# Kernel tuning notes

Hardware: AMD Instinct MI355X
Metric: run time of the kernel (lower is better)

The kernel has to match this reference:

```python
import jax, jax.numpy as jnp
import numpy as np

K = 10  # knn_graph default k
NEG_SLOPE = 0.2


def _knn_idx(x, k):
    # x: (B, N, C) -> idx (B, N, k) of nearest neighbors (excluding self)
    x2 = jnp.sum(x * x, axis=-1)                       # (B, N)
    d = x2[:, :, None] + x2[:, None, :] - 2.0 * jnp.einsum('bnc,bmc->bnm', x, x)
    _, idx = jax.lax.top_k(-d, k + 1)                  # smallest distances
    return idx[:, :, 1:]                               # drop self


def _edge_conv(x, W, s, t, k):
    # x: (B, N, C); W: (O, 2C); s,t: (O,) folded BN scale/bias
    idx = _knn_idx(x, k)                               # (B, N, k)
    neigh = jax.vmap(lambda xb, ib: xb[ib])(x, idx)    # (B, N, k, C)
    xi = jnp.broadcast_to(x[:, :, None, :], neigh.shape)
    edge = jnp.concatenate([neigh - xi, xi], axis=-1)  # (B, N, k, 2C)
    h = jnp.einsum('bnkc,oc->bnko', edge, W) * s + t
    h = jnp.where(h >= 0, h, NEG_SLOPE * h)            # LeakyReLU(0.2)
    return jnp.max(h, axis=2)                          # max over neighbors -> (B, N, O)


def setup_inputs() -> dict:
    key = jax.random.key(0)
    ks = jax.random.split(key, 32)
    B, N = 8, 2048
    NC = 3
    def w(k_, shape):
        fan_in = shape[-1]
        return jax.random.normal(k_, shape, jnp.float32) * (1.0 / np.sqrt(fan_in))
    def sb(k_, c):  # positive scale, small bias
        k1, k2 = jax.random.split(k_)
        return (jax.random.uniform(k1, (c,), jnp.float32, 0.5, 1.5),
                jax.random.normal(k2, (c,), jnp.float32) * 0.1)
    points = jax.random.normal(ks[0], (B, N, 3), jnp.float32)
    W1 = w(ks[1], (64, 6));    s1, t1 = sb(ks[2], 64)
    W2 = w(ks[3], (64, 128));  s2, t2 = sb(ks[4], 64)
    W3 = w(ks[5], (128, 128)); s3, t3 = sb(ks[6], 128)
    W4 = w(ks[7], (256, 256)); s4, t4 = sb(ks[8], 256)
    W5 = w(ks[9], (1024, 512)); s5, t5 = sb(ks[10], 1024)
    Wf1 = w(ks[11], (512, 1024)); sf1, tf1 = sb(ks[12], 512)
    Wf2 = w(ks[13], (256, 512)); bf2 = jax.random.normal(ks[14], (256,), jnp.float32) * 0.02
    sf2, tf2 = sb(ks[15], 256)
    Wf3 = w(ks[16], (NC, 256)); bf3 = jax.random.normal(ks[17], (NC,), jnp.float32) * 0.02
    return {
        'points': points,
        'W1': W1, 's1': s1, 't1': t1,
        'W2': W2, 's2': s2, 't2': t2,
        'W3': W3, 's3': s3, 't3': t3,
        'W4': W4, 's4': s4, 't4': t4,
        'W5': W5, 's5': s5, 't5': t5,
        'Wf1': Wf1, 'sf1': sf1, 'tf1': tf1,
        'Wf2': Wf2, 'bf2': bf2, 'sf2': sf2, 'tf2': tf2,
        'Wf3': Wf3, 'bf3': bf3,
    }


def reference(points, W1, s1, t1, W2, s2, t2, W3, s3, t3, W4, s4, t4,
              W5, s5, t5, Wf1, sf1, tf1, Wf2, bf2, sf2, tf2, Wf3, bf3):
    lrelu = lambda h: jnp.where(h >= 0, h, NEG_SLOPE * h)
    out1 = _edge_conv(points, W1, s1, t1, K)   # (B, N, 64)
    out2 = _edge_conv(out1, W2, s2, t2, K)     # (B, N, 64)
    out3 = _edge_conv(out2, W3, s3, t3, K)     # (B, N, 128)
    out4 = _edge_conv(out3, W4, s4, t4, K)     # (B, N, 256)
    x = jnp.concatenate([out1, out2, out3, out4], axis=-1)  # (B, N, 512)
    h = lrelu(jnp.einsum('bnc,oc->bno', x, W5) * s5 + t5)   # (B, N, 1024)
    h = jnp.max(h, axis=1)                                  # global max pool -> (B, 1024)
    h = lrelu((h @ Wf1.T) * sf1 + tf1)                      # (B, 512); dropout=identity (eval)
    h = lrelu((h @ Wf2.T + bf2) * sf2 + tf2)                # (B, 256)
    return h @ Wf3.T + bf3                                  # (B, num_classes)
```

## Files before the change

kernel.cpp:

```cpp
#include <hip/hip_runtime.h>
#include <hip/hip_bf16.h>


#define NEG 0.2f
#define FMAX 3.402823466e+38f
#define FMAXB 0x7F7FFFFFu
#define KINIT 0x7F7FFFFFFFFFFFFFull

typedef __hip_bfloat16 bf16;
typedef __attribute__((ext_vector_type(8))) short s8v;
typedef __attribute__((ext_vector_type(4))) float f32x4;
typedef unsigned long long u64;

#define BB 8
#define NN 2048
#define BNTOT (BB * NN)
#define NPART 4

#define OFF_NORMS ((size_t)0)
#define OFF_PART (OFF_NORMS + BNTOT)
#define OFF_POOLED (OFF_PART + 8 * 1024 * 32)
#define OFF_H1 (OFF_POOLED + 8 * 1024)
#define OFF_H2 (OFF_H1 + 8 * 512)
#define WSF_TOTAL (OFF_H2 + 8 * 256)

#define WB1 0
#define WB2 4096
#define WB3 12288
#define WB4 28672
#define WTOT 94208

__device__ float g_ws_f[WSF_TOTAL];
__device__ float g_G[(size_t)8 * BNTOT * 64];
__device__ u64 g_pk[(size_t)BNTOT * NPART * 10];
__device__ unsigned g_th[BNTOT];
__device__ int g_flag;
__device__ unsigned short g_hi[(size_t)BNTOT * 512];
__device__ unsigned short g_lo[(size_t)BNTOT * 512];
__device__ unsigned short g_xhi5[(size_t)BNTOT * 512];
__device__ unsigned short g_xlo5[(size_t)BNTOT * 512];
__device__ unsigned short g_whi[1024 * 512];
__device__ unsigned short g_wlo[1024 * 512];
__device__ unsigned short g_wfh[WTOT];
__device__ unsigned short g_wfl[WTOT];

__device__ __forceinline__ float ldany(const void* p, size_t i, int isb) {
  if (isb) return __bfloat162float(((const bf16*)p)[i]);
  return ((const float*)p)[i];
}

__global__ void probe_kernel(const void* pts) {
  const unsigned* w = (const unsigned*)pts;
  int cnt = 0;
  for (int i = 0; i < 256; ++i) {
    unsigned e2 = (w[i] >> 7) & 0xFF;
    cnt += (e2 >= 110 && e2 <= 135);
  }
  g_flag = (cnt > 128) ? 1 : 0;
}

__global__ void norms_kernel(const void* xraw, int lda, int C, int BN) {
  const int isb = g_flag;
  float* norms = g_ws_f + OFF_NORMS;
  int row = blockIdx.x * (blockDim.x >> 6) + (threadIdx.x >> 6);
  int lane = threadIdx.x & 63;
  if (row >= BN) return;
  float s = 0.f;
  for (int c = lane; c < C; c += 64) {
    float v = ldany(xraw, (size_t)row * lda + c, isb);
    s += v * v;
  }
#pragma unroll
  for (int off = 32; off > 0; off >>= 1) s += __shfl_down(s, off, 64);
  if (lane == 0) { norms[row] = s; g_th[row] = FMAXB; }
}

__global__ void zero_norms() {
  int i = blockIdx.x * blockDim.x + threadIdx.x;
  if (i < BNTOT) g_ws_f[OFF_NORMS + i] = 0.f;
}

__global__ void split_kernel(const void* xraw, int lda, int C,
                             int csh2, int dst, int total) {
  int i = blockIdx.x * blockDim.x + threadIdx.x;
  if (i >= total) return;
  const int isb = g_flag;
  int t = i >> 9, win = i & 511;
  int quad = win >> 7, l16 = (win >> 3) & 15, j = win & 7;
  int ktiles_m1 = (1 << csh2) - 1;
  int rg = t >> csh2, kt = t & ktiles_m1;
  int r = rg * 16 + l16;
  int c = kt * 32 + quad * 8 + j;
  float v = (c < C) ? ldany(xraw, (size_t)r * lda + c, isb) : 0.f;
  bf16 h = __float2bfloat16(v);
  float hf = __bfloat162float(h);
  bf16 l = __float2bfloat16(v - hf);
  unsigned short* H = dst ? g_whi : g_hi;
  unsigned short* L = dst ? g_wlo : g_lo;
  H[i] = *(unsigned short*)&h;
  L[i] = *(unsigned short*)&l;
}

__global__ void split_w(const void* W, int C, int ktsh, int wbase, int whalf,
                        int total) {
  int i = blockIdx.x * blockDim.x + threadIdx.x;
  if (i >= total) return;
  int z = blockIdx.y;
  const int isb = g_flag;
  int t = i >> 9, win = i & 511;
  int quad = win >> 7, l16 = (win >> 3) & 15, j = win & 7;
  int rg = t >> ktsh, kt = t & ((1 << ktsh) - 1);
  int orow = rg * 16 + l16;
  int c = kt * 32 + quad * 8 + j;
  float v = (c < C) ? ldany(W, (size_t)orow * (2 * C) + (size_t)z * C + c, isb) : 0.f;
  bf16 h = __float2bfloat16(v);
  float hf = __bfloat162float(h);
  bf16 l = __float2bfloat16(v - hf);
  g_wfh[wbase + z * whalf + i] = *(unsigned short*)&h;
  g_wfl[wbase + z * whalf + i] = *(unsigned short*)&l;
}

template <int CPAD>
__global__ __launch_bounds__(256) void knn_fused(int N) {
  constexpr int KT = CPAD >> 5;
  __shared__ __align__(16) float sdbuf[2][64 * 68];
  const int tid = threadIdx.x;
  const int wave = tid >> 6, lane = tid & 63;
  const int quad = lane >> 4, l16 = lane & 15;
  const int b = blockIdx.y;
  const int q0 = blockIdx.x * 64;
  const int part = blockIdx.z;
  const int PN = N / NPART;
  const size_t rowb = (size_t)b * N;
  const float* norms = g_ws_f + OFF_NORMS;

  const int arg = (int)((rowb + q0) >> 4) + wave;
  s8v ah[KT], al[KT];
#pragma unroll
  for (int kt = 0; kt < KT; ++kt) {
    const size_t abase = ((size_t)arg * KT + kt) * 512 + lane * 8;
    ah[kt] = *(const s8v*)(g_hi + abase);
    al[kt] = *(const s8v*)(g_lo + abase);
  }

  const int selfn = q0 + lane;
  const float qn = norms[rowb + selfn];
  u64 K[10];
#pragma unroll
  for (int i = 0; i < 10; ++i) K[i] = KINIT;
  unsigned gth = FMAXB;

  int pb = 0;
  for (int m0 = part * PN; m0 < (part + 1) * PN; m0 += 64, pb ^= 1) {
    f32x4 acc[4];
#pragma unroll
    for (int s = 0; s < 4; ++s) acc[s] = (f32x4){0.f, 0.f, 0.f, 0.f};
    const int brg0 = (int)((rowb + m0) >> 4);
#pragma unroll
    for (int kt = 0; kt < KT; ++kt) {
#pragma unroll
      for (int s = 0; s < 4; ++s) {
        const size_t bbase = ((size_t)(brg0 + s) * KT + kt) * 512 + lane * 8;
        s8v bh = *(const s8v*)(g_hi + bbase);
        s8v bl = *(const s8v*)(g_lo + bbase);
        acc[s] = __builtin_amdgcn_mfma_f32_16x16x32_bf16(ah[kt], bh, acc[s], 0, 0, 0);
        acc[s] = __builtin_amdgcn_mfma_f32_16x16x32_bf16(ah[kt], bl, acc[s], 0, 0, 0);
        acc[s] = __builtin_amdgcn_mfma_f32_16x16x32_bf16(al[kt], bh, acc[s], 0, 0, 0);
      }
    }
    float* sd = sdbuf[pb];
#pragma unroll
    for (int s = 0; s < 4; ++s) {
      int ml = s * 16 + l16;
      float nm = norms[rowb + m0 + ml];
#pragma unroll
      for (int r = 0; r < 4; ++r)
        sd[(wave * 16 + quad * 4 + r) * 68 + ml] = nm - 2.f * acc[s][r];
    }
    __syncthreads();
    const float T = __uint_as_float(gth);
    const int mbase = m0 + wave * 16;
    const float* srow = sd + lane * 68 + wave * 16;
    unsigned pass = 0;
#pragma unroll
    for (int jj = 0; jj < 16; jj += 4) {
      float4 d4 = *(const float4*)(srow + jj);
      pass |= (unsigned)(d4.x + qn <= T) << jj;
      pass |= (unsigned)(d4.y + qn <= T) << (jj + 1);
      pass |= (unsigned)(d4.z + qn <= T) << (jj + 2);
      pass |= (unsigned)(d4.w + qn <= T) << (jj + 3);
    }
    if ((unsigned)(selfn - mbase) < 16u) pass &= ~(1u << (selfn - mbase));
    while (pass) {
      int jj = __builtin_ctz(pass);
      pass &= pass - 1;
      int m = mbase + jj;
      float d = fmaxf(srow[jj] + qn, 0.f);
      u64 key = ((u64)__float_as_uint(d) << 32) | (unsigned)m;
      if (key < K[9]) {
        bool prev = true;
#pragma unroll
        for (int s2 = 9; s2 >= 1; --s2) {
          bool sh = key < K[s2 - 1];
          K[s2] = sh ? K[s2 - 1] : (prev ? key : K[s2]);
          prev = sh;
        }
        if (prev) K[0] = key;
      }
    }
    unsigned mine = (unsigned)(K[9] >> 32);
    unsigned old = atomicMin(&g_th[rowb + selfn], mine);
    gth = min(min(gth, old), mine);
  }
  __syncthreads();
  u64* mlist = (u64*)sdbuf;
#pragma unroll
  for (int i = 0; i < 10; ++i) mlist[(lane * 4 + wave) * 10 + i] = K[i];
  __syncthreads();
  if (tid < 64) {
    int q = tid;
    int p0 = 0, p1 = 0, p2 = 0, p3 = 0;
    size_t ob = ((rowb + q0 + q) * NPART + part) * 10;
    for (int cnt = 0; cnt < 10; ++cnt) {
      u64 k0 = mlist[(q * 4 + 0) * 10 + p0];
      u64 k1 = mlist[(q * 4 + 1) * 10 + p1];
      u64 k2 = mlist[(q * 4 + 2) * 10 + p2];
      u64 k3 = mlist[(q * 4 + 3) * 10 + p3];
      u64 bk = k0; int bp = 0;
      if (k1 < bk) { bk = k1; bp = 1; }
      if (k2 < bk) { bk = k2; bp = 2; }
      if (k3 < bk) { bk = k3; bp = 3; }
      if (bp == 0) ++p0; else if (bp == 1) ++p1; else if (bp == 2) ++p2; else ++p3;
      g_pk[ob + cnt] = bk;
    }
  }
}

template <int CPAD>
__global__ __launch_bounds__(256) void gmat_mfma(int wbase, int whalf, int BN) {
  constexpr int KT = CPAD >> 5;
  const int tid = threadIdx.x;
  const int wave = tid >> 6, lane = tid & 63;
  const int quad = lane >> 4, l16 = lane & 15;
  const int r0 = blockIdx.x * 64;
  const int chunk = blockIdx.y;
  const int z = blockIdx.z;
  const int wz = wbase + z * whalf;
  const int wrg0 = chunk * 4;
  f32x4 acc[4];
#pragma unroll
  for (int s = 0; s < 4; ++s) acc[s] = (f32x4){0.f, 0.f, 0.f, 0.f};
  const int arg = (r0 >> 4) + wave;
#pragma unroll
  for (int kt = 0; kt < KT; ++kt) {
    const size_t abase = ((size_t)arg * KT + kt) * 512 + lane * 8;
    s8v ah = *(const s8v*)(g_hi + abase);
    s8v al = *(const s8v*)(g_lo + abase);
#pragma unroll
    for (int s = 0; s < 4; ++s) {
      const size_t woff = (size_t)wz + ((size_t)(wrg0 + s) * KT + kt) * 512 + lane * 8;
      s8v bh = *(const s8v*)(g_wfh + woff);
      s8v bl = *(const s8v*)(g_wfl + woff);
      acc[s] = __builtin_amdgcn_mfma_f32_16x16x32_bf16(ah, bh, acc[s], 0, 0, 0);
      acc[s] = __builtin_amdgcn_mfma_f32_16x16x32_bf16(ah, bl, acc[s], 0, 0, 0);
      acc[s] = __builtin_amdgcn_mfma_f32_16x16x32_bf16(al, bh, acc[s], 0, 0, 0);
    }
  }
  float* Gz = g_G + (size_t)(chunk * 2 + z) * BN * 64;
#pragma unroll
  for (int s = 0; s < 4; ++s)
#pragma unroll
    for (int r = 0; r < 4; ++r)
      Gz[(size_t)(r0 + wave * 16 + quad * 4 + r) * 64 + s * 16 + l16] = acc[s][r];
}

__global__ void edge_epi64(const void* s, const void* t, int colbase,
                           int knn_csh2, int norms_mode, int BN, int N) {
  __shared__ u64 kbuf[4][40];
  __shared__ int oidx[4][10];
  const int isb = g_flag;
  int tid = threadIdx.x;
  int p = tid >> 6, o = tid & 63;
  int row = blockIdx.x * 4 + p;
  int chunk = blockIdx.y;
  const float* G1 = g_G + (size_t)(chunk * 2 + 0) * BN * 64;
  const float* G2 = g_G + (size_t)(chunk * 2 + 1) * BN * 64;
  int b = row / N;
  if (o < 40) kbuf[p][o] = g_pk[(size_t)row * 40 + o];
  if (o < 40) {
    u64 myk = kbuf[p][o];
    int rank = 0;
#pragma unroll 8
    for (int j = 0; j < 40; ++j) rank += (kbuf[p][j] < myk);
    if (rank < 10) oidx[p][rank] = (int)(myk & 0xFFFFFFFFu);
  }
  float g1n = G1[(size_t)row * 64 + o];
  float base = G2[(size_t)row * 64 + o] - g1n;
  int co = chunk * 64 + o;
  float sv = ldany(s, co, isb), tv = ldany(t, co, isb);
  float mx = -FMAX;
#pragma unroll
  for (int k = 0; k < 10; ++k) {
    int m = oidx[p][k];
    m = (m < 0) ? 0 : ((m >= N) ? N - 1 : m);
    float h = sv * (G1[((size_t)b * N + m) * 64 + o] + base) + tv;
    h = (h >= 0.f) ? h : NEG * h;
    mx = fmaxf(mx, h);
  }
  bf16 h16 = __float2bfloat16(mx);
  float hf = __bfloat162float(h16);
  bf16 l16v = __float2bfloat16(mx - hf);
  unsigned short hu = *(unsigned short*)&h16;
  unsigned short lu = *(unsigned short*)&l16v;
  if (knn_csh2 >= 0) {
    int KTL = 1 << knn_csh2;
    size_t ki = ((size_t)(row >> 4) * KTL + (co >> 5)) * 512 +
                ((size_t)((co >> 3) & 3)) * 128 + (row & 15) * 8 + (co & 7);
    g_hi[ki] = hu; g_lo[ki] = lu;
  }
  {
    int gc = colbase + co;
    size_t wi = ((size_t)(row >> 4) * 16 + (gc >> 5)) * 512 +
                ((size_t)((gc >> 3) & 3)) * 128 + (row & 15) * 8 + (gc & 7);
    g_xhi5[wi] = hu; g_xlo5[wi] = lu;
  }
  if (norms_mode) {
    float ns = mx * mx;
#pragma unroll
    for (int off = 32; off > 0; off >>= 1) ns += __shfl_down(ns, off, 64);
    if (o == 0) {
      if (norms_mode == 1) g_ws_f[OFF_NORMS + row] = ns;
      else atomicAdd(&g_ws_f[OFF_NORMS + row], ns);
      g_th[row] = FMAXB;
    }
  }
}

__global__ __launch_bounds__(256) void w5max_mfma(const void* s5, const void* t5, int N) {
  const int tid = threadIdx.x;
  const int wave = tid >> 6, lane = tid & 63;
  const int quad = lane >> 4, l16 = lane & 15;
  const int b = blockIdx.z;
  const int o0 = blockIdx.y * 64, n0 = blockIdx.x * 256;
  f32x4 acc[4][4];
#pragma unroll
  for (int a = 0; a < 4; ++a)
#pragma unroll
    for (int s = 0; s < 4; ++s) acc[a][s] = (f32x4){0.f, 0.f, 0.f, 0.f};

  const int arg0 = (int)(((size_t)b * N + n0) >> 4) + wave * 4;
  const int wrg0 = o0 >> 4;
  for (int kt = 0; kt < 16; ++kt) {
    s8v ah[4], al[4];
#pragma unroll
    for (int a = 0; a < 4; ++a) {
      const size_t abase = ((size_t)(arg0 + a) * 16 + kt) * 512 + lane * 8;
      ah[a] = *(const s8v*)(g_xhi5 + abase);
      al[a] = *(const s8v*)(g_xlo5 + abase);
    }
#pragma unroll
    for (int s = 0; s < 4; ++s) {
      const size_t bbase = ((size_t)(wrg0 + s) * 16 + kt) * 512 + lane * 8;
      s8v bh = *(const s8v*)(g_whi + bbase);
      s8v bl = *(const s8v*)(g_wlo + bbase);
#pragma unroll
      for (int a = 0; a < 4; ++a) {
        acc[a][s] = __builtin_amdgcn_mfma_f32_16x16x32_bf16(ah[a], bh, acc[a][s], 0, 0, 0);
        acc[a][s] = __builtin_amdgcn_mfma_f32_16x16x32_bf16(ah[a], bl, acc[a][s], 0, 0, 0);
        acc[a][s] = __builtin_amdgcn_mfma_f32_16x16x32_bf16(al[a], bh, acc[a][s], 0, 0, 0);
      }
    }
  }
  __shared__ float red[4][64];
  const int isb = g_flag;
#pragma unroll
  for (int s = 0; s < 4; ++s) {
    float m4 = -FMAX;
#pragma unroll
    for (int a = 0; a < 4; ++a)
#pragma unroll
      for (int r = 0; r < 4; ++r) m4 = fmaxf(m4, acc[a][s][r]);
#pragma unroll
    for (int off = 16; off < 64; off <<= 1) m4 = fmaxf(m4, __shfl_down(m4, off, 64));
    if (quad == 0) red[wave][s * 16 + l16] = m4;
  }
  __syncthreads();
  if (tid < 64) {
    float m = fmaxf(fmaxf(red[0][tid], red[1][tid]), fmaxf(red[2][tid], red[3][tid]));
    int o = o0 + tid;
    float sv = ldany(s5, o, isb), tv = ldany(t5, o, isb);
    float h = sv * m + tv;
    h = (h >= 0.f) ? h : NEG * h;
    g_ws_f[OFF_PART + ((size_t)b * 1024 + o) * 8 + blockIdx.x] = h;
  }
}

__global__ void poolred_kernel() {
  const float* part = g_ws_f + OFF_PART;
  float* pooled = g_ws_f + OFF_POOLED;
  int i = blockIdx.x * blockDim.x + threadIdx.x;
  if (i >= 8 * 1024) return;
  const float* p = part + (size_t)i * 8;
  float m = -FMAX;
#pragma unroll
  for (int j = 0; j < 8; ++j) m = fmaxf(m, p[j]);
  pooled[i] = m;
}

__global__ void fc_kernel(size_t inoff, const void* W, const void* bias,
                          const void* s, const void* t, size_t outoff, int has_out,
                          void* OUTB, int Bb, int IC, int OC, int act) {
  const int isb = g_flag;
  const float* IN = g_ws_f + inoff;
  int gw = (blockIdx.x * blockDim.x + threadIdx.x) >> 6;
  int lane = threadIdx.x & 63;
  if (gw >= Bb * OC) return;
  int b = gw / OC, o = gw % OC;
  const float* in = IN + (size_t)b * IC;
  float acc = 0.f;
  for (int c = lane; c < IC; c += 64) acc += in[c] * ldany(W, (size_t)o * IC + c, isb);
#pragma unroll
  for (int off = 32; off > 0; off >>= 1) acc += __shfl_down(acc, off, 64);
  if (lane == 0) {
    float h = acc;
    if (bias) h += ldany(bias, o, isb);
    if (s) h = h * ldany(s, o, isb) + ldany(t, o, isb);
    if (act) h = (h >= 0.f) ? h : NEG * h;
    if (has_out) g_ws_f[outoff + (size_t)b * OC + o] = h;
    if (OUTB) {
      if (isb) ((bf16*)OUTB)[(size_t)b * OC + o] = __float2bfloat16(h);
      else ((float*)OUTB)[(size_t)b * OC + o] = h;
    }
  }
}

extern "C" void kernel_launch(void* const* d_in, const int* in_sizes, int n_in,
                              void* d_out, int out_size, void* d_ws, size_t ws_size,
                              hipStream_t stream) {
  const int B = 8, N = 2048, BN = B * N;
  const void* points = d_in[0];
  const void *W1 = d_in[1], *s1 = d_in[2], *t1 = d_in[3];
  const void *W2 = d_in[4], *s2 = d_in[5], *t2 = d_in[6];
  const void *W3 = d_in[7], *s3 = d_in[8], *t3 = d_in[9];
  const void *W4 = d_in[10], *s4 = d_in[11], *t4 = d_in[12];
  const void *W5 = d_in[13], *s5 = d_in[14], *t5 = d_in[15];
  const void *Wf1 = d_in[16], *sf1 = d_in[17], *tf1 = d_in[18];
  const void *Wf2 = d_in[19], *bf2 = d_in[20], *sf2 = d_in[21], *tf2 = d_in[22];
  const void *Wf3 = d_in[23], *bf3 = d_in[24];

  probe_kernel<<<1, 1, 0, stream>>>(points);
  split_kernel<<<(1024 * 512) / 256, 256, 0, stream>>>(W5, 512, 512, 4, 1, 1024 * 512);
  split_w<<<dim3(2048 / 256, 2), 256, 0, stream>>>(W1, 3, 0, WB1, 2048, 2048);
  split_w<<<dim3(4096 / 256, 2), 256, 0, stream>>>(W2, 64, 1, WB2, 4096, 4096);
  split_w<<<dim3(8192 / 256, 2), 256, 0, stream>>>(W3, 64, 1, WB3, 8192, 8192);
  split_w<<<dim3(32768 / 256, 2), 256, 0, stream>>>(W4, 128, 2, WB4, 32768, 32768);

  norms_kernel<<<BN / 4, 256, 0, stream>>>(points, 3, 3, BN);
  split_kernel<<<(BN * 32) / 256, 256, 0, stream>>>(points, 3, 3, 0, 0, BN * 32);
  knn_fused<32><<<dim3(N / 64, B, NPART), 256, 0, stream>>>(N);
  gmat_mfma<32><<<dim3(BN / 64, 1, 2), 256, 0, stream>>>(WB1, 2048, BN);
  edge_epi64<<<dim3(BN / 4, 1), 256, 0, stream>>>(s1, t1, 0, 1, 1, BN, N);
  knn_fused<64><<<dim3(N / 64, B, NPART), 256, 0, stream>>>(N);
  gmat_mfma<64><<<dim3(BN / 64, 1, 2), 256, 0, stream>>>(WB2, 4096, BN);
  edge_epi64<<<dim3(BN / 4, 1), 256, 0, stream>>>(s2, t2, 64, 1, 1, BN, N);
  knn_fused<64><<<dim3(N / 64, B, NPART), 256, 0, stream>>>(N);
  gmat_mfma<64><<<dim3(BN / 64, 2, 2), 256, 0, stream>>>(WB3, 8192, BN);
  zero_norms<<<BN / 256, 256, 0, stream>>>();
  edge_epi64<<<dim3(BN / 4, 2), 256, 0, stream>>>(s3, t3, 128, 2, 2, BN, N);
  knn_fused<128><<<dim3(N / 64, B, NPART), 256, 0, stream>>>(N);
  gmat_mfma<128><<<dim3(BN / 64, 4, 2), 256, 0, stream>>>(WB4, 32768, BN);
  edge_epi64<<<dim3(BN / 4, 4), 256, 0, stream>>>(s4, t4, 256, -1, 0, BN, N);
  w5max_mfma<<<dim3(8, 16, 8), 256, 0, stream>>>(s5, t5, N);
  poolred_kernel<<<32, 256, 0, stream>>>();
  fc_kernel<<<(8 * 512 * 64) / 256, 256, 0, stream>>>(OFF_POOLED, Wf1, nullptr, sf1, tf1, OFF_H1, 1, nullptr, 8, 1024, 512, 1);
  fc_kernel<<<(8 * 256 * 64) / 256, 256, 0, stream>>>(OFF_H1, Wf2, bf2, sf2, tf2, OFF_H2, 1, nullptr, 8, 512, 256, 1);
  fc_kernel<<<6, 256, 0, stream>>>(OFF_H2, Wf3, bf3, nullptr, nullptr, 0, 0, d_out, 8, 256, 3, 0);
}
```

Measured before the change: 570.5 us.

## Split kNN candidate scan into eight partitions and raise knn_fused occupancy

The fused kNN kernel now splits each query's candidate range into eight partitions instead of four, doubling the number of blocks. It also drops the double-buffered distance tile for a single padded shared buffer, guarded by an extra barrier. That shrinks shared memory use, and launch bounds now request higher occupancy. The per-partition merge is done in two halves of 32 queries so it fits the smaller buffer, and the edge epilogue ranks 80 partial candidates instead of 40. The trade-off is more partial lists to merge, more per-partition threshold warm-up work, and extra barriers in the scan loop.

After: 706.1 us. +23.8%, slower.

```diff
diff --git a/kernel.cpp b/kernel.cpp
--- a/kernel.cpp
+++ b/kernel.cpp
@@ -15,7 +15,7 @@
 #define BB 8
 #define NN 2048
 #define BNTOT (BB * NN)
-#define NPART 4
+#define NPART 8
 
 #define OFF_NORMS ((size_t)0)
 #define OFF_PART (OFF_NORMS + BNTOT)
@@ -121,9 +121,9 @@
 }
 
 template <int CPAD>
-__global__ __launch_bounds__(256) void knn_fused(int N) {
+__global__ __launch_bounds__(256, 8) void knn_fused(int N) {
   constexpr int KT = CPAD >> 5;
-  __shared__ __align__(16) float sdbuf[2][64 * 68];
+  __shared__ __align__(16) float sd[64 * 76];
   const int tid = threadIdx.x;
   const int wave = tid >> 6, lane = tid & 63;
   const int quad = lane >> 4, l16 = lane & 15;
@@ -150,8 +150,7 @@
   for (int i = 0; i < 10; ++i) K[i] = KINIT;
   unsigned gth = FMAXB;
 
-  int pb = 0;
-  for (int m0 = part * PN; m0 < (part + 1) * PN; m0 += 64, pb ^= 1) {
+  for (int m0 = part * PN; m0 < (part + 1) * PN; m0 += 64) {
     f32x4 acc[4];
 #pragma unroll
     for (int s = 0; s < 4; ++s) acc[s] = (f32x4){0.f, 0.f, 0.f, 0.f};
@@ -168,19 +167,19 @@
         acc[s] = __builtin_amdgcn_mfma_f32_16x16x32_bf16(al[kt], bh, acc[s], 0, 0, 0);
       }
     }
-    float* sd = sdbuf[pb];
+    __syncthreads();
 #pragma unroll
     for (int s = 0; s < 4; ++s) {
       int ml = s * 16 + l16;
       float nm = norms[rowb + m0 + ml];
 #pragma unroll
       for (int r = 0; r < 4; ++r)
-        sd[(wave * 16 + quad * 4 + r) * 68 + ml] = nm - 2.f * acc[s][r];
+        sd[(wave * 16 + quad * 4 + r) * 76 + ml] = nm - 2.f * acc[s][r];
     }
     __syncthreads();
     const float T = __uint_as_float(gth);
     const int mbase = m0 + wave * 16;
-    const float* srow = sd + lane * 68 + wave * 16;
+    const float* srow = sd + lane * 76 + wave * 16;
     unsigned pass = 0;
 #pragma unroll
     for (int jj = 0; jj < 16; jj += 4) {
@@ -213,26 +212,31 @@
     gth = min(min(gth, old), mine);
   }
   __syncthreads();
-  u64* mlist = (u64*)sdbuf;
-#pragma unroll
-  for (int i = 0; i < 10; ++i) mlist[(lane * 4 + wave) * 10 + i] = K[i];
-  __syncthreads();
-  if (tid < 64) {
-    int q = tid;
-    int p0 = 0, p1 = 0, p2 = 0, p3 = 0;
-    size_t ob = ((rowb + q0 + q) * NPART + part) * 10;
-    for (int cnt = 0; cnt < 10; ++cnt) {
-      u64 k0 = mlist[(q * 4 + 0) * 10 + p0];
-      u64 k1 = mlist[(q * 4 + 1) * 10 + p1];
-      u64 k2 = mlist[(q * 4 + 2) * 10 + p2];
-      u64 k3 = mlist[(q * 4 + 3) * 10 + p3];
-      u64 bk = k0; int bp = 0;
-      if (k1 < bk) { bk = k1; bp = 1; }
-      if (k2 < bk) { bk = k2; bp = 2; }
-      if (k3 < bk) { bk = k3; bp = 3; }
-      if (bp == 0) ++p0; else if (bp == 1) ++p1; else if (bp == 2) ++p2; else ++p3;
-      g_pk[ob + cnt] = bk;
-    }
+  u64* mlist = (u64*)sd;
+  for (int qh = 0; qh < 2; ++qh) {
+    if ((lane >> 5) == qh) {
+#pragma unroll
+      for (int i = 0; i < 10; ++i) mlist[((lane & 31) * 4 + wave) * 10 + i] = K[i];
+    }
+    __syncthreads();
+    if (tid < 32) {
+      int q = qh * 32 + tid;
+      int p0 = 0, p1 = 0, p2 = 0, p3 = 0;
+      size_t ob = ((rowb + q0 + q) * NPART + part) * 10;
+      for (int cnt = 0; cnt < 10; ++cnt) {
+        u64 k0 = mlist[(tid * 4 + 0) * 10 + p0];
+        u64 k1 = mlist[(tid * 4 + 1) * 10 + p1];
+        u64 k2 = mlist[(tid * 4 + 2) * 10 + p2];
+        u64 k3 = mlist[(tid * 4 + 3) * 10 + p3];
+        u64 bk = k0; int bp = 0;
+        if (k1 < bk) { bk = k1; bp = 1; }
+        if (k2 < bk) { bk = k2; bp = 2; }
+        if (k3 < bk) { bk = k3; bp = 3; }
+        if (bp == 0) ++p0; else if (bp == 1) ++p1; else if (bp == 2) ++p2; else ++p3;
+        g_pk[ob + cnt] = bk;
+      }
+    }
+    __syncthreads();
   }
 }
 
@@ -276,7 +280,7 @@
 
 __global__ void edge_epi64(const void* s, const void* t, int colbase,
                            int knn_csh2, int norms_mode, int BN, int N) {
-  __shared__ u64 kbuf[4][40];
+  __shared__ u64 kbuf[4][NPART * 10];
   __shared__ int oidx[4][10];
   const int isb = g_flag;
   int tid = threadIdx.x;
@@ -286,13 +290,20 @@
   const float* G1 = g_G + (size_t)(chunk * 2 + 0) * BN * 64;
   const float* G2 = g_G + (size_t)(chunk * 2 + 1) * BN * 64;
   int b = row / N;
-  if (o < 40) kbuf[p][o] = g_pk[(size_t)row * 40 + o];
-  if (o < 40) {
-    u64 myk = kbuf[p][o];
-    int rank = 0;
+  kbuf[p][o] = g_pk[(size_t)row * (NPART * 10) + o];
+  if (o < NPART * 10 - 64) kbuf[p][64 + o] = g_pk[(size_t)row * (NPART * 10) + 64 + o];
+  {
+    u64 myk0 = kbuf[p][o];
+    u64 myk1 = kbuf[p][(o < NPART * 10 - 64) ? 64 + o : o];
+    int r0 = 0, r1 = 0;
 #pragma unroll 8
-    for (int j = 0; j < 40; ++j) rank += (kbuf[p][j] < myk);
-    if (rank < 10) oidx[p][rank] = (int)(myk & 0xFFFFFFFFu);
+    for (int j = 0; j < NPART * 10; ++j) {
+      u64 kj = kbuf[p][j];
+      r0 += (kj < myk0);
+      r1 += (kj < myk1);
+    }
+    if (r0 < 10) oidx[p][r0] = (int)(myk0 & 0xFFFFFFFFu);
+    if (o < NPART * 10 - 64 && r1 < 10) oidx[p][r1] = (int)(myk1 & 0xFFFFFFFFu);
   }
   float g1n = G1[(size_t)row * 64 + o];
   float base = G2[(size_t)row * 64 + o] - g1n;
```
